# Kernel tuning notes

Hardware: AMD Instinct MI355X
Metric: run time of the kernel (lower is better)

Reference implementation:

```python
import jax, jax.numpy as jnp
import numpy as np

B, C, H, W = 2, 256, 360, 360
N1 = N2 = 1024


def setup_inputs() -> dict:
    key = jax.random.key(0)
    ks = jax.random.split(key, 12)
    s = 0.02
    feature = jax.random.normal(ks[0], (B, C, H, W), dtype=jnp.float32)
    # midx rows: [batch_idx, h, w]; frame 0 centers and frame 1 centers
    idx1 = jnp.stack([
        jnp.zeros((N1,), dtype=jnp.int32),
        jax.random.randint(ks[1], (N1,), 0, H, dtype=jnp.int32),
        jax.random.randint(ks[2], (N1,), 0, W, dtype=jnp.int32),
    ])
    idx2 = jnp.stack([
        jnp.ones((N2,), dtype=jnp.int32),
        jax.random.randint(ks[3], (N2,), 0, H, dtype=jnp.int32),
        jax.random.randint(ks[4], (N2,), 0, W, dtype=jnp.int32),
    ])
    w1 = jax.random.normal(ks[5], (256, 256), dtype=jnp.float32) * s
    b1 = jnp.zeros((256,), dtype=jnp.float32)
    w2 = jax.random.normal(ks[6], (256, 128), dtype=jnp.float32) * s
    b2 = jnp.zeros((128,), dtype=jnp.float32)
    w3 = jax.random.normal(ks[7], (128, 32), dtype=jnp.float32) * s
    b3 = jnp.zeros((32,), dtype=jnp.float32)
    w4 = jax.random.normal(ks[8], (32, 1), dtype=jnp.float32) * s
    b4 = jnp.zeros((1,), dtype=jnp.float32)
    return {"feature": feature, "idx1": idx1, "idx2": idx2,
            "w1": w1, "b1": b1, "w2": w2, "b2": b2,
            "w3": w3, "b3": b3, "w4": w4, "b4": b4}


def reference(feature, idx1, idx2, w1, b1, w2, b2, w3, b3, w4, b4):
    # feature: [B,C,H,W] -> [B,H,W,C] (torch .permute(0,2,3,1))
    feat = jnp.transpose(feature, (0, 2, 3, 1))

    def project(midx):
        # irregular gather of per-center features: [N, C]
        x = feat[midx[0], midx[1], midx[2]]
        h = jax.nn.relu(x @ w1 + b1)          # [N, 256]
        return jax.nn.relu(h @ w2 + b2)       # [N, 128]

    f1 = project(idx1)                        # [N1, D]
    f2 = project(idx2)                        # [N2, D]
    # laplacian_dists: broadcast outer difference [N1, N2, D]
    diff = f1[:, None, :] - f2[None, :, :]
    # out_layer = linear_last(D, 32, 1): Linear -> ReLU -> Linear
    h = jax.nn.relu(jnp.einsum('mnd,dk->mnk', diff, w3) + b3)
    out = jnp.einsum('mnk,ko->mno', h, w4) + b4
    return out[..., 0]                        # [N1, N2] similarity
```

## Files before the change

kernel.cpp:

```cpp
#include <hip/hip_runtime.h>

#define NPTS 1024
#define NC 256
#define NH 360
#define NW 360
#define NHW (NH * NW)
#define NCHW (NC * NHW)

typedef float v2f __attribute__((ext_vector_type(2)));

__global__ __launch_bounds__(256) void gather_kernel(
    const float* __restrict__ feature,
    const int* __restrict__ idx1,
    const int* __restrict__ idx2,
    float4* __restrict__ Xq)
{
    const int c = threadIdx.x;
    const int quad = blockIdx.x;
    const int base = quad * 4;
    const int col0 = base & (NPTS - 1);
    const int* idx = (base < NPTS) ? idx1 : idx2;
    const int4 bb4 = *(const int4*)(idx + col0);
    const int4 hh4 = *(const int4*)(idx + NPTS + col0);
    const int4 ww4 = *(const int4*)(idx + 2 * NPTS + col0);
    const size_t coff = (size_t)c * NHW;
    float4 v;
    v.x = __builtin_nontemporal_load(
              feature + (size_t)bb4.x * NCHW + coff + (size_t)(hh4.x * NW + ww4.x));
    v.y = __builtin_nontemporal_load(
              feature + (size_t)bb4.y * NCHW + coff + (size_t)(hh4.y * NW + ww4.y));
    v.z = __builtin_nontemporal_load(
              feature + (size_t)bb4.z * NCHW + coff + (size_t)(hh4.z * NW + ww4.z));
    v.w = __builtin_nontemporal_load(
              feature + (size_t)bb4.w * NCHW + coff + (size_t)(hh4.w * NW + ww4.w));
    Xq[(size_t)quad * 256 + c] = v;
}

__global__ __launch_bounds__(256) void mlp_kernel(
    const float4* __restrict__ Xq,
    const float* __restrict__ w1, const float* __restrict__ b1,
    const float* __restrict__ w2, const float* __restrict__ b2,
    const float* __restrict__ w3, const float* __restrict__ b3,
    float* __restrict__ pq)
{
    __shared__ float4 H1s[256];
    __shared__ float4 F2s[128];

    const int t = threadIdx.x;
    const int quad = blockIdx.x;
    const int base = quad * 4;
    const float4* __restrict__ Xr = Xq + (size_t)quad * 256;

    {
        float4 acc = make_float4(0.f, 0.f, 0.f, 0.f);
        #pragma unroll 8
        for (int c = 0; c < 256; ++c) {
            const float4 a = Xr[c];
            const float wv = w1[c * 256 + t];
            acc.x = fmaf(a.x, wv, acc.x);
            acc.y = fmaf(a.y, wv, acc.y);
            acc.z = fmaf(a.z, wv, acc.z);
            acc.w = fmaf(a.w, wv, acc.w);
        }
        const float bj = b1[t];
        float4 h;
        h.x = fmaxf(acc.x + bj, 0.f);
        h.y = fmaxf(acc.y + bj, 0.f);
        h.z = fmaxf(acc.z + bj, 0.f);
        h.w = fmaxf(acc.w + bj, 0.f);
        H1s[t] = h;
    }
    __syncthreads();

    {
        const int j = t & 127;
        const int ph = t >> 7;
        const float* H1f = (const float*)H1s;
        float2 acc = make_float2(0.f, 0.f);
        #pragma unroll 8
        for (int c = 0; c < 256; ++c) {
            const float wv = w2[c * 128 + j];
            const float2 a = *(const float2*)&H1f[c * 4 + 2 * ph];
            acc.x = fmaf(a.x, wv, acc.x);
            acc.y = fmaf(a.y, wv, acc.y);
        }
        const float bj = b2[j];
        float* F2f = (float*)F2s;
        F2f[j * 4 + 2 * ph + 0] = fmaxf(acc.x + bj, 0.f);
        F2f[j * 4 + 2 * ph + 1] = fmaxf(acc.y + bj, 0.f);
    }
    __syncthreads();

    if (t < 128) {
        const int j = t & 31;
        const int g = t >> 5;
        const float* F2f = (const float*)F2s;
        float acc = 0.f;
        #pragma unroll 8
        for (int c = 0; c < 128; ++c)
            acc = fmaf(F2f[c * 4 + g], w3[c * 32 + j], acc);
        const int point = base + g;
        const float val = (point < NPTS) ? acc : (b3[j] - acc);
        pq[(size_t)point * 32 + j] = val;
    }
}

#define MT 8

__global__ __launch_bounds__(256) void pair_kernel(
    const float* __restrict__ pq,
    const float* __restrict__ w4,
    const float* __restrict__ b4,
    float* __restrict__ out)
{
    const int tid = threadIdx.x;
    const int n = blockIdx.x * 256 + tid;
    const int m0 = blockIdx.y * MT;

    v2f q[16];
    const float4* q4 = (const float4*)(pq + (size_t)(NPTS + n) * 32);
    #pragma unroll
    for (int k8 = 0; k8 < 8; ++k8) {
        float4 v = q4[k8];
        q[2 * k8 + 0] = (v2f){v.x, v.y};
        q[2 * k8 + 1] = (v2f){v.z, v.w};
    }
    const float b4v = b4[0];
    const v2f zero = {0.f, 0.f};

    #pragma unroll
    for (int mm = 0; mm < MT; ++mm) {
        const v2f* Pm = (const v2f*)(pq + (size_t)(m0 + mm) * 32);
        const v2f* w4v = (const v2f*)w4;
        v2f acc = {b4v, 0.f};
        #pragma unroll
        for (int k2 = 0; k2 < 16; ++k2) {
            v2f tv = Pm[k2] + q[k2];
            v2f rv = __builtin_elementwise_max(tv, zero);
            acc = __builtin_elementwise_fma(w4v[k2], rv, acc);
        }
        out[(size_t)(m0 + mm) * 1024 + n] = acc.x + acc.y;
    }
}

extern "C" void kernel_launch(void* const* d_in, const int* in_sizes, int n_in,
                              void* d_out, int out_size, void* d_ws, size_t ws_size,
                              hipStream_t stream) {
    const float* feature = (const float*)d_in[0];
    const int*   idx1    = (const int*)d_in[1];
    const int*   idx2    = (const int*)d_in[2];
    const float* w1      = (const float*)d_in[3];
    const float* b1      = (const float*)d_in[4];
    const float* w2      = (const float*)d_in[5];
    const float* b2      = (const float*)d_in[6];
    const float* w3      = (const float*)d_in[7];
    const float* b3      = (const float*)d_in[8];
    const float* w4      = (const float*)d_in[9];
    const float* b4      = (const float*)d_in[10];
    float* out = (float*)d_out;

    float*  pq = (float*)d_ws;
    float4* Xq = (float4*)((char*)d_ws + 256 * 1024);

    gather_kernel<<<512, 256, 0, stream>>>(feature, idx1, idx2, Xq);
    mlp_kernel<<<512, 256, 0, stream>>>(Xq, w1, b1, w2, b2, w3, b3, pq);
    pair_kernel<<<dim3(4, 128), 256, 0, stream>>>(pq, w4, b4, out);
}
```

Measured before the change: 363.1 us.

## Fuse feature gather into MLP kernel via async global-to-LDS loads

Removes the separate gather kernel and its workspace round trip. The MLP kernel now issues direct global-to-LDS loads for the four gathered points, split into two pairs. It computes the first pair's layers while the second pair's loads are still in flight, using manual waitcnt barriers. Layer 2 is split across both half-blocks with a partial-sum combine step. This saves one launch and the intermediate write and read, but relies on hand-counted vmcnt waits, which are fragile.

```diff
diff --git a/kernel.cpp b/kernel.cpp
--- a/kernel.cpp
+++ b/kernel.cpp
@@ -9,100 +9,133 @@
 
 typedef float v2f __attribute__((ext_vector_type(2)));
 
-__global__ __launch_bounds__(256) void gather_kernel(
+__device__ __forceinline__ void gload_lds4(const float* g, float* lds) {
+    __builtin_amdgcn_global_load_lds(
+        (const __attribute__((address_space(1))) void*)g,
+        (__attribute__((address_space(3))) void*)lds, 4, 0, 0);
+}
+
+#define BAR_LDS() do { asm volatile("s_waitcnt lgkmcnt(0)" ::: "memory"); \
+                       __builtin_amdgcn_s_barrier(); } while (0)
+#define BAR_ALL() do { asm volatile("s_waitcnt vmcnt(0) lgkmcnt(0)" ::: "memory"); \
+                       __builtin_amdgcn_s_barrier(); } while (0)
+#define BAR_VM2() do { asm volatile("s_waitcnt vmcnt(2)" ::: "memory"); \
+                       __builtin_amdgcn_s_barrier(); } while (0)
+
+__global__ __launch_bounds__(256) void mlp_kernel(
     const float* __restrict__ feature,
     const int* __restrict__ idx1,
     const int* __restrict__ idx2,
-    float4* __restrict__ Xq)
-{
-    const int c = threadIdx.x;
-    const int quad = blockIdx.x;
-    const int base = quad * 4;
-    const int col0 = base & (NPTS - 1);
-    const int* idx = (base < NPTS) ? idx1 : idx2;
-    const int4 bb4 = *(const int4*)(idx + col0);
-    const int4 hh4 = *(const int4*)(idx + NPTS + col0);
-    const int4 ww4 = *(const int4*)(idx + 2 * NPTS + col0);
-    const size_t coff = (size_t)c * NHW;
-    float4 v;
-    v.x = __builtin_nontemporal_load(
-              feature + (size_t)bb4.x * NCHW + coff + (size_t)(hh4.x * NW + ww4.x));
-    v.y = __builtin_nontemporal_load(
-              feature + (size_t)bb4.y * NCHW + coff + (size_t)(hh4.y * NW + ww4.y));
-    v.z = __builtin_nontemporal_load(
-              feature + (size_t)bb4.z * NCHW + coff + (size_t)(hh4.z * NW + ww4.z));
-    v.w = __builtin_nontemporal_load(
-              feature + (size_t)bb4.w * NCHW + coff + (size_t)(hh4.w * NW + ww4.w));
-    Xq[(size_t)quad * 256 + c] = v;
-}
-
-__global__ __launch_bounds__(256) void mlp_kernel(
-    const float4* __restrict__ Xq,
     const float* __restrict__ w1, const float* __restrict__ b1,
     const float* __restrict__ w2, const float* __restrict__ b2,
     const float* __restrict__ w3, const float* __restrict__ b3,
     float* __restrict__ pq)
 {
-    __shared__ float4 H1s[256];
-    __shared__ float4 F2s[128];
-
-    const int t = threadIdx.x;
-    const int quad = blockIdx.x;
-    const int base = quad * 4;
-    const float4* __restrict__ Xr = Xq + (size_t)quad * 256;
+    __shared__ __align__(16) float Xs[2][512];
+    __shared__ __align__(16) float H1s[512];
+    __shared__ v2f  P2s[128][2];
+    __shared__ float F2s[256];
+
+    const int tid = threadIdx.x;
+    const int l   = tid & 63;
+    const int wv  = tid >> 6;
+    const int base = blockIdx.x * 4;
+
+    const int col0 = base & (NPTS - 1);
+    const int* idx = (base < NPTS) ? idx1 : idx2;
+    const int4 bb = *(const int4*)(idx + col0);
+    const int4 hh = *(const int4*)(idx + NPTS + col0);
+    const int4 ww = *(const int4*)(idx + 2 * NPTS + col0);
+    const size_t off0 = (size_t)bb.x * NCHW + (size_t)(hh.x * NW + ww.x);
+    const size_t off1 = (size_t)bb.y * NCHW + (size_t)(hh.y * NW + ww.y);
+    const size_t off2 = (size_t)bb.z * NCHW + (size_t)(hh.z * NW + ww.z);
+    const size_t off3 = (size_t)bb.w * NCHW + (size_t)(hh.w * NW + ww.w);
 
     {
-        float4 acc = make_float4(0.f, 0.f, 0.f, 0.f);
+        const int pt = l & 1;
+        const int cl = l >> 1;
+        const size_t oA = pt ? off1 : off0;
+        #pragma unroll
+        for (int k = 0; k < 2; ++k) {
+            const int chunk = wv * 2 + k;
+            const int c = chunk * 32 + cl;
+            gload_lds4(feature + oA + (size_t)c * NHW, &Xs[0][chunk * 64]);
+        }
+        const size_t oB = pt ? off3 : off2;
+        #pragma unroll
+        for (int k = 0; k < 2; ++k) {
+            const int chunk = wv * 2 + k;
+            const int c = chunk * 32 + cl;
+            gload_lds4(feature + oB + (size_t)c * NHW, &Xs[1][chunk * 64]);
+        }
+    }
+
+    auto layer1 = [&](const float* Xp) {
+        float a0 = 0.f, a1 = 0.f;
         #pragma unroll 8
-        for (int c = 0; c < 256; ++c) {
-            const float4 a = Xr[c];
-            const float wv = w1[c * 256 + t];
-            acc.x = fmaf(a.x, wv, acc.x);
-            acc.y = fmaf(a.y, wv, acc.y);
-            acc.z = fmaf(a.z, wv, acc.z);
-            acc.w = fmaf(a.w, wv, acc.w);
-        }
-        const float bj = b1[t];
-        float4 h;
-        h.x = fmaxf(acc.x + bj, 0.f);
-        h.y = fmaxf(acc.y + bj, 0.f);
-        h.z = fmaxf(acc.z + bj, 0.f);
-        h.w = fmaxf(acc.w + bj, 0.f);
-        H1s[t] = h;
-    }
-    __syncthreads();
-
-    {
-        const int j = t & 127;
-        const int ph = t >> 7;
-        const float* H1f = (const float*)H1s;
-        float2 acc = make_float2(0.f, 0.f);
+        for (int c2 = 0; c2 < 128; ++c2) {
+            const float4 x = *(const float4*)&Xp[c2 * 4];
+            const float wa = w1[(2 * c2) * 256 + tid];
+            const float wb = w1[(2 * c2 + 1) * 256 + tid];
+            a0 = fmaf(x.x, wa, a0); a1 = fmaf(x.y, wa, a1);
+            a0 = fmaf(x.z, wb, a0); a1 = fmaf(x.w, wb, a1);
+        }
+        const float bj = b1[tid];
+        H1s[2 * tid + 0] = fmaxf(a0 + bj, 0.f);
+        H1s[2 * tid + 1] = fmaxf(a1 + bj, 0.f);
+    };
+    auto layer2a = [&]() {
+        const int j = tid & 127;
+        const int chh = tid >> 7;
+        float a0 = 0.f, a1 = 0.f;
         #pragma unroll 8
-        for (int c = 0; c < 256; ++c) {
-            const float wv = w2[c * 128 + j];
-            const float2 a = *(const float2*)&H1f[c * 4 + 2 * ph];
-            acc.x = fmaf(a.x, wv, acc.x);
-            acc.y = fmaf(a.y, wv, acc.y);
-        }
-        const float bj = b2[j];
-        float* F2f = (float*)F2s;
-        F2f[j * 4 + 2 * ph + 0] = fmaxf(acc.x + bj, 0.f);
-        F2f[j * 4 + 2 * ph + 1] = fmaxf(acc.y + bj, 0.f);
-    }
-    __syncthreads();
-
-    if (t < 128) {
-        const int j = t & 31;
-        const int g = t >> 5;
-        const float* F2f = (const float*)F2s;
-        float acc = 0.f;
-        #pragma unroll 8
-        for (int c = 0; c < 128; ++c)
-            acc = fmaf(F2f[c * 4 + g], w3[c * 32 + j], acc);
-        const int point = base + g;
-        const float val = (point < NPTS) ? acc : (b3[j] - acc);
-        pq[(size_t)point * 32 + j] = val;
-    }
+        for (int c2 = 0; c2 < 64; ++c2) {
+            const int c = chh * 128 + 2 * c2;
+            const float4 x = *(const float4*)&H1s[2 * c];
+            const float wa = w2[c * 128 + j];
+            const float wb = w2[(c + 1) * 128 + j];
+            a0 = fmaf(x.x, wa, a0); a1 = fmaf(x.y, wa, a1);
+            a0 = fmaf(x.z, wb, a0); a1 = fmaf(x.w, wb, a1);
+        }
+        P2s[j][chh] = (v2f){a0, a1};
+    };
+    auto combine2 = [&]() {
+        if (tid < 128) {
+            const v2f s = P2s[tid][0] + P2s[tid][1];
+            const float bj = b2[tid];
+            F2s[2 * tid + 0] = fmaxf(s.x + bj, 0.f);
+            F2s[2 * tid + 1] = fmaxf(s.y + bj, 0.f);
+        }
+    };
+    auto layer3 = [&](int u) {
+        if (tid < 64) {
+            const int j = tid & 31;
+            const int pt = tid >> 5;
+            float acc = 0.f;
+            #pragma unroll 8
+            for (int c = 0; c < 128; ++c)
+                acc = fmaf(F2s[2 * c + pt], w3[c * 32 + j], acc);
+            const int point = base + 2 * u + pt;
+            const float val = (base < NPTS) ? acc : (b3[j] - acc);
+            pq[(size_t)point * 32 + j] = val;
+        }
+    };
+
+    BAR_VM2();
+    layer1(Xs[0]);
+    BAR_LDS();
+    layer2a();
+    BAR_LDS();
+    combine2();
+    BAR_ALL();
+    layer3(0);
+    layer1(Xs[1]);
+    BAR_LDS();
+    layer2a();
+    BAR_LDS();
+    combine2();
+    BAR_LDS();
+    layer3(1);
 }
 
 #define MT 8
@@ -159,10 +192,10 @@
     const float* b4      = (const float*)d_in[10];
     float* out = (float*)d_out;
 
-    float*  pq = (float*)d_ws;
-    float4* Xq = (float4*)((char*)d_ws + 256 * 1024);
-
-    gather_kernel<<<512, 256, 0, stream>>>(feature, idx1, idx2, Xq);
-    mlp_kernel<<<512, 256, 0, stream>>>(Xq, w1, b1, w2, b2, w3, b3, pq);
+    float* pq = (float*)d_ws;
+
+    mlp_kernel<<<512, 256, 0, stream>>>(
+        feature, idx1, idx2, w1, b1, w2, b2, w3, b3, pq);
+
     pair_kernel<<<dim3(4, 128), 256, 0, stream>>>(pq, w4, b4, out);
 }
```

Result: no change. 361.1 us (-0.5%).
